# Performance work log

Hardware: AMD Instinct MI355X
Metric: run time of the kernel (lower is better)

## Reference

```python
import jax, jax.numpy as jnp
import numpy as np

IC = 64   # inter_channels
S = 3     # num_subset_S
ST = 2    # num_subset_T


def _bn(x, g, b):
    # BatchNorm2d in eval mode with running_mean=0, running_var=1, eps=1e-5
    return x * (g / jnp.sqrt(1.0 + 1e-5))[:, None, None] + b[:, None, None]


def _c1(x, W, b):
    # 1x1 Conv2d over (N, C, T, V)
    return jnp.einsum('oc,nctv->notv', W, x) + b[None, :, None, None]


def setup_inputs() -> dict:
    key = jax.random.key(0)
    ks = iter(jax.random.split(key, 40))
    r = lambda sh: jax.random.normal(next(ks), sh, dtype=jnp.float32) * 0.05
    N, C, T, V = 64, 128, 64, 25
    d = {}
    d['x'] = jax.random.normal(next(ks), (N, C, T, V), dtype=jnp.float32)
    d['W_ins'] = r((2 * S * IC, C)); d['b_ins'] = r((2 * S * IC,))
    d['alphas'] = jnp.ones((1, S, 1, 1), jnp.float32)
    d['att0s'] = jnp.full((1, S, V, V), 1.0 / V, jnp.float32)
    d['W_outs'] = r((C, S * C)); d['b_outs'] = r((C,))
    d['g_outs'] = jnp.ones((C,), jnp.float32) + r((C,)); d['be_outs'] = r((C,))
    d['W_ffs'] = r((C, C)); d['b_ffs'] = r((C,))
    d['g_ffs'] = jnp.ones((C,), jnp.float32) + r((C,)); d['be_ffs'] = r((C,))
    d['W_int'] = r((4 * ST * IC, C)); d['b_int'] = r((4 * ST * IC,))
    d['alphat_b'] = jnp.ones((1, ST, 1, 1), jnp.float32)
    d['alphat_f'] = jnp.ones((1, ST, 1, 1), jnp.float32)
    d['W_outt'] = r((C, 2 * ST * C)); d['b_outt'] = r((C,))
    d['g_outt'] = jnp.ones((C,), jnp.float32) + r((C,)); d['be_outt'] = r((C,))
    d['W_fft'] = r((C, C)); d['b_fft'] = r((C,))
    d['g_fft'] = jnp.ones((C,), jnp.float32) + r((C,)); d['be_fft'] = r((C,))
    d['W_tcn'] = r((C, C, 7, 1)); d['b_tcn'] = r((C,))
    d['g_tcn'] = jnp.ones((C,), jnp.float32) + r((C,)); d['be_tcn'] = r((C,))
    return d


def reference(x, W_ins, b_ins, alphas, att0s, W_outs, b_outs, g_outs, be_outs,
              W_ffs, b_ffs, g_ffs, be_ffs, W_int, b_int, alphat_b, alphat_f,
              W_outt, b_outt, g_outt, be_outt, W_fft, b_fft, g_fft, be_fft,
              W_tcn, b_tcn, g_tcn, be_tcn):
    N, C, T, V = x.shape
    lrelu = lambda a: jax.nn.leaky_relu(a, 0.1)

    # ---- spatial attention ----
    qk = _c1(x, W_ins, b_ins).reshape(N, 2 * S, IC, T, V)
    q, k = qk[:, :S], qk[:, S:]
    att = jnp.tanh(jnp.einsum('nsctu,nsctv->nsuv', q, k) / (IC * T)) * alphas + att0s
    y = jnp.einsum('nctu,nsuv->nsctv', x, att).reshape(N, S * C, T, V)
    y = lrelu(x + _bn(_c1(y, W_outs, b_outs), g_outs, be_outs))   # out_nets + residual
    y = lrelu(x + _bn(_c1(y, W_ffs, b_ffs), g_ffs, be_ffs))       # ff_nets + residual (downs2 = identity)

    # ---- directed temporal attention ----
    bm = jnp.triu(jnp.ones((T, T), x.dtype))  # backward mask
    fm = bm.T                                  # forward mask (tril)
    qk = _c1(y, W_int, b_int).reshape(N, 4 * ST, IC, T, V)
    q_f, q_b = qk[:, :ST], qk[:, ST:2 * ST]
    k_f, k_b = qk[:, 2 * ST:3 * ST], qk[:, 3 * ST:]
    att_b = jnp.tanh(jnp.einsum('nsctv,nscqv->nstq', q_b, k_b) / (IC * V)) * alphat_b * bm
    att_f = jnp.tanh(jnp.einsum('nsctv,nscqv->nstq', q_f, k_f) / (IC * V)) * alphat_f * fm
    z_f = jnp.einsum('nctv,nstq->nscqv', y, att_f).reshape(N, ST * C, T, V)
    z_b = jnp.einsum('nctv,nstq->nscqv', y, att_b).reshape(N, ST * C, T, V)
    z = jnp.concatenate([z_f, z_b], axis=1)                        # (N, 2*ST*C, T, V)
    z = lrelu(y + _bn(_c1(z, W_outt, b_outt), g_outt, be_outt))    # out_nett + residual
    z = lrelu(y + _bn(_c1(z, W_fft, b_fft), g_fft, be_fft))        # ff_nett + residual

    # ---- TCN extension: (7,1) temporal conv + BN + residual ----
    z1 = jax.lax.conv_general_dilated(z, W_tcn, (1, 1), ((3, 3), (0, 0)),
                                      dimension_numbers=('NCHW', 'OIHW', 'NCHW'))
    z1 = _bn(z1 + b_tcn[None, :, None, None] - b_tcn[None, :, None, None] + b_tcn[None, :, None, None], g_tcn, be_tcn) if False else _bn(z1 + b_tcn[None, :, None, None], g_tcn, be_tcn)
    z = lrelu(z + z1)
    return z
```

## Files before the change

### kernel.cpp

```cpp
#include <hip/hip_runtime.h>

#define BNSC 0.99999500003749963f

typedef _Float16 f16;
typedef _Float16 f16x8 __attribute__((ext_vector_type(8)));
typedef float    f32x4 __attribute__((ext_vector_type(4)));

static __device__ __forceinline__ float lrelu_f(float a) { return a >= 0.0f ? a : 0.1f * a; }

static __device__ __forceinline__ void xcd_swz(int& bx, int& by, int& bz) {
    const int GX = gridDim.x, GY = gridDim.y, GZ = gridDim.z;
    if (((GX * GZ) & 7) == 0) {
        const int lin = blockIdx.x + GX * (blockIdx.y + GY * blockIdx.z);
        const int xcd = lin & 7;
        const int rest = lin >> 3;
        by = rest % GY;
        const int g = (rest / GY) * 8 + xcd;
        bx = g % GX;
        bz = g / GX;
    } else {
        bx = blockIdx.x; by = blockIdx.y; bz = blockIdx.z;
    }
}

__global__ __launch_bounds__(256) void prep_w_k(
    const float* __restrict__ Wins, const float* __restrict__ Wouts,
    const float* __restrict__ Wffs, const float* __restrict__ Wint,
    const float* __restrict__ Woutt, const float* __restrict__ Wfft,
    const float* __restrict__ Wtcn, f16* __restrict__ dst)
{
    int i = blockIdx.x * 256 + threadIdx.x;
    int o = 0;
    if (i < 49152) { dst[o + i] = (f16)Wins[i];  return; } i -= 49152; o += 49152;
    if (i < 49152) { dst[o + i] = (f16)Wouts[i]; return; } i -= 49152; o += 49152;
    if (i < 16384) { dst[o + i] = (f16)Wffs[i];  return; } i -= 16384; o += 16384;
    if (i < 65536) { dst[o + i] = (f16)Wint[i];  return; } i -= 65536; o += 65536;
    if (i < 65536) { dst[o + i] = (f16)Woutt[i]; return; } i -= 65536; o += 65536;
    if (i < 16384) { dst[o + i] = (f16)Wfft[i];  return; } i -= 16384; o += 16384;
    if (i < 114688) {
        int tau = i / 16384, rem = i - tau * 16384;
        dst[o + i] = (f16)Wtcn[(size_t)rem * 7 + tau];
    }
}

__global__ __launch_bounds__(256) void x_to_T_k(const float* __restrict__ x,
                                                f16* __restrict__ xT, f16* __restrict__ xBp)
{
    __shared__ float L[64 * 68];
    const int n = blockIdx.z, tv0 = blockIdx.x * 64, c0 = blockIdx.y * 64;
    const int tid = threadIdx.x;
    const int cc = tid >> 4, tv4 = (tid & 15) * 4;
    f16* xBn = xBp + (size_t)n * 262144;
    #pragma unroll
    for (int p = 0; p < 4; ++p) {
        const int c = cc + p * 16;
        float4 v = *(const float4*)&x[((size_t)n * 128 + c0 + c) * 1600 + tv0 + tv4];
        *(float4*)&L[c * 68 + tv4] = v;
        const float vv[4] = {v.x, v.y, v.z, v.w};
        #pragma unroll
        for (int e = 0; e < 4; ++e) {
            const int tvg = tv0 + tv4 + e;
            const int t = tvg / 25, u = tvg - t * 25;
            xBn[(size_t)(c0 + c) * 2048 + t * 32 + u] = (f16)vv[e];
        }
    }
    __syncthreads();
    const int tv = tid & 63, cb = (tid >> 6) * 16;
    f16x8 o0, o1;
    #pragma unroll
    for (int i = 0; i < 8; ++i) o0[i] = (f16)L[(cb + i) * 68 + tv];
    #pragma unroll
    for (int i = 0; i < 8; ++i) o1[i] = (f16)L[(cb + 8 + i) * 68 + tv];
    f16* dst = &xT[((size_t)n * 1600 + tv0 + tv) * 128 + c0 + cb];
    *(f16x8*)dst = o0;
    *(f16x8*)(dst + 8) = o1;
}

__global__ __launch_bounds__(256) void T_to_out_k(const f16* __restrict__ oT, float* __restrict__ out)
{
    __shared__ float L[128 * 69];
    const int n = blockIdx.z, tv0 = blockIdx.x * 64;
    const int tid = threadIdx.x;
    #pragma unroll
    for (int p = 0; p < 4; ++p) {
        int idx = tid + p * 256;
        int tv = idx >> 4, c8 = (idx & 15) * 8;
        f16x8 v = *(const f16x8*)&oT[((size_t)n * 1600 + tv0 + tv) * 128 + c8];
        #pragma unroll
        for (int i = 0; i < 8; ++i) L[(c8 + i) * 69 + tv] = (float)v[i];
    }
    __syncthreads();
    const int c = tid >> 1, tvb = (tid & 1) * 32;
    #pragma unroll
    for (int j = 0; j < 8; ++j) {
        float4 o;
        o.x = L[c * 69 + tvb + j * 4 + 0];
        o.y = L[c * 69 + tvb + j * 4 + 1];
        o.z = L[c * 69 + tvb + j * 4 + 2];
        o.w = L[c * 69 + tvb + j * 4 + 3];
        *(float4*)&out[((size_t)n * 128 + c) * 1600 + tv0 + tvb + j * 4] = o;
    }
}

template<int EPI>
__global__ __launch_bounds__(256) void gemm_t_k(
    const f16* __restrict__ A,
    const f16* __restrict__ W,
    const float* __restrict__ bias,
    const float* __restrict__ g, const float* __restrict__ be,
    const f16* __restrict__ res,
    f16* __restrict__ out,
    int K, int M)
{
    __shared__ __align__(16) char smem[34816];
    f16* As = (f16*)smem;
    f16* Bs = (f16*)(smem + 17408);
    float* Ss = (float*)smem;
    int bx, by, bz;
    xcd_swz(bx, by, bz);
    const int n = bz, tv0 = bx * 64, m0 = by * 64;
    const int tid = threadIdx.x;
    const int w = tid >> 6, lane = tid & 63;
    const int wr = w >> 1, wc = w & 1;
    const int lg = lane >> 4, lr = lane & 15;
    const int srow = tid >> 3, scol = (tid & 7) * 16;
    const f16* An = A + (size_t)n * 1600 * K;
    f32x4 acc[2][2] = {};

    for (int k0 = 0; k0 < K; k0 += 128) {
        const f16* ar0 = An + (size_t)(tv0 + srow) * K + k0 + scol;
        const f16* ar1 = An + (size_t)(tv0 + srow + 32) * K + k0 + scol;
        const f16* br0 = W + (size_t)(m0 + srow) * K + k0 + scol;
        const f16* br1 = W + (size_t)(m0 + srow + 32) * K + k0 + scol;
        uint4 a0 = *(const uint4*)ar0, a1 = *(const uint4*)(ar0 + 8);
        uint4 a2 = *(const uint4*)ar1, a3 = *(const uint4*)(ar1 + 8);
        uint4 b0 = *(const uint4*)br0, b1 = *(const uint4*)(br0 + 8);
        uint4 b2 = *(const uint4*)br1, b3 = *(const uint4*)(br1 + 8);
        __syncthreads();
        *(uint4*)&As[srow * 136 + scol] = a0;
        *(uint4*)&As[srow * 136 + scol + 8] = a1;
        *(uint4*)&As[(srow + 32) * 136 + scol] = a2;
        *(uint4*)&As[(srow + 32) * 136 + scol + 8] = a3;
        *(uint4*)&Bs[srow * 136 + scol] = b0;
        *(uint4*)&Bs[srow * 136 + scol + 8] = b1;
        *(uint4*)&Bs[(srow + 32) * 136 + scol] = b2;
        *(uint4*)&Bs[(srow + 32) * 136 + scol + 8] = b3;
        __syncthreads();
        #pragma unroll
        for (int kb = 0; kb < 128; kb += 32) {
            f16x8 af0 = *(const f16x8*)&As[(wr * 32 + lr) * 136 + kb + lg * 8];
            f16x8 af1 = *(const f16x8*)&As[(wr * 32 + 16 + lr) * 136 + kb + lg * 8];
            f16x8 bf0 = *(const f16x8*)&Bs[(wc * 32 + lr) * 136 + kb + lg * 8];
            f16x8 bf1 = *(const f16x8*)&Bs[(wc * 32 + 16 + lr) * 136 + kb + lg * 8];
            acc[0][0] = __builtin_amdgcn_mfma_f32_16x16x32_f16(af0, bf0, acc[0][0], 0, 0, 0);
            acc[0][1] = __builtin_amdgcn_mfma_f32_16x16x32_f16(af0, bf1, acc[0][1], 0, 0, 0);
            acc[1][0] = __builtin_amdgcn_mfma_f32_16x16x32_f16(af1, bf0, acc[1][0], 0, 0, 0);
            acc[1][1] = __builtin_amdgcn_mfma_f32_16x16x32_f16(af1, bf1, acc[1][1], 0, 0, 0);
        }
        __syncthreads();
    }
    #pragma unroll
    for (int fi = 0; fi < 2; ++fi)
        #pragma unroll
        for (int fj = 0; fj < 2; ++fj)
            #pragma unroll
            for (int rr = 0; rr < 4; ++rr)
                Ss[(wr * 32 + fi * 16 + lg * 4 + rr) * 68 + wc * 32 + fj * 16 + lr] = acc[fi][fj][rr];
    __syncthreads();
    const int tvl = tid >> 2, mq = (tid & 3) * 16;
    const int tv = tv0 + tvl;
    const int m  = m0 + mq;
    float vals[16];
    #pragma unroll
    for (int j = 0; j < 4; ++j)
        *(float4*)&vals[j * 4] = *(const float4*)&Ss[tvl * 68 + mq + j * 4];
    float bi[16];
    #pragma unroll
    for (int j = 0; j < 4; ++j) *(float4*)&bi[j * 4] = *(const float4*)&bias[m + j * 4];
    if (EPI == 1) {
        float gg[16], bb[16];
        #pragma unroll
        for (int j = 0; j < 4; ++j) {
            *(float4*)&gg[j * 4] = *(const float4*)&g[m + j * 4];
            *(float4*)&bb[j * 4] = *(const float4*)&be[m + j * 4];
        }
        const f16* rp = res + ((size_t)n * 1600 + tv) * M + m;
        f16x8 r0 = *(const f16x8*)rp;
        f16x8 r1 = *(const f16x8*)(rp + 8);
        #pragma unroll
        for (int j = 0; j < 16; ++j) {
            float r = (float)((j < 8) ? r0[j & 7] : r1[j & 7]);
            vals[j] = lrelu_f(r + (vals[j] + bi[j]) * (gg[j] * BNSC) + bb[j]);
        }
    } else {
        #pragma unroll
        for (int j = 0; j < 16; ++j) vals[j] += bi[j];
    }
    f16x8 o0, o1;
    #pragma unroll
    for (int j = 0; j < 8; ++j) { o0[j] = (f16)vals[j]; o1[j] = (f16)vals[8 + j]; }
    f16* op = out + ((size_t)n * 1600 + tv) * M + m;
    *(f16x8*)op = o0;
    *(f16x8*)(op + 8) = o1;
}

__global__ __launch_bounds__(256) void tcn_T_k(
    const f16* __restrict__ z2T,
    const f16* __restrict__ W7,
    const float* __restrict__ bias, const float* __restrict__ g,
    const float* __restrict__ be, f16* __restrict__ outT)
{
    __shared__ __align__(16) char smem[34816];
    f16* As = (f16*)smem;
    f16* Bs = (f16*)(smem + 17408);
    float* Ss = (float*)smem;
    int bx, by, bz;
    xcd_swz(bx, by, bz);
    const int n = bz, tv0 = bx * 64, m0 = by * 64;
    const int tid = threadIdx.x;
    const int w = tid >> 6, lane = tid & 63;
    const int wr = w >> 1, wc = w & 1;
    const int lg = lane >> 4, lr = lane & 15;
    const int srow = tid >> 3, scol = (tid & 7) * 16;
    const f16* Zn = z2T + (size_t)n * 204800;
    f32x4 acc[2][2] = {};

    for (int tau = 0; tau < 7; ++tau) {
        const int shift = (tau - 3) * 25;
        const f16* Wt = W7 + tau * 16384;
        const int gr0 = tv0 + srow + shift;
        const int gr1 = gr0 + 32;
        uint4 a0 = make_uint4(0,0,0,0), a1 = a0, a2 = a0, a3 = a0;
        if (gr0 >= 0 && gr0 < 1600) {
            const f16* p = Zn + (size_t)gr0 * 128 + scol;
            a0 = *(const uint4*)p; a1 = *(const uint4*)(p + 8);
        }
        if (gr1 >= 0 && gr1 < 1600) {
            const f16* p = Zn + (size_t)gr1 * 128 + scol;
            a2 = *(const uint4*)p; a3 = *(const uint4*)(p + 8);
        }
        const f16* br0 = Wt + (size_t)(m0 + srow) * 128 + scol;
        const f16* br1 = Wt + (size_t)(m0 + srow + 32) * 128 + scol;
        uint4 b0 = *(const uint4*)br0, b1 = *(const uint4*)(br0 + 8);
        uint4 b2 = *(const uint4*)br1, b3 = *(const uint4*)(br1 + 8);
        __syncthreads();
        *(uint4*)&As[srow * 136 + scol] = a0;
        *(uint4*)&As[srow * 136 + scol + 8] = a1;
        *(uint4*)&As[(srow + 32) * 136 + scol] = a2;
        *(uint4*)&As[(srow + 32) * 136 + scol + 8] = a3;
        *(uint4*)&Bs[srow * 136 + scol] = b0;
        *(uint4*)&Bs[srow * 136 + scol + 8] = b1;
        *(uint4*)&Bs[(srow + 32) * 136 + scol] = b2;
        *(uint4*)&Bs[(srow + 32) * 136 + scol + 8] = b3;
        __syncthreads();
        #pragma unroll
        for (int kb = 0; kb < 128; kb += 32) {
            f16x8 af0 = *(const f16x8*)&As[(wr * 32 + lr) * 136 + kb + lg * 8];
            f16x8 af1 = *(const f16x8*)&As[(wr * 32 + 16 + lr) * 136 + kb + lg * 8];
            f16x8 bf0 = *(const f16x8*)&Bs[(wc * 32 + lr) * 136 + kb + lg * 8];
            f16x8 bf1 = *(const f16x8*)&Bs[(wc * 32 + 16 + lr) * 136 + kb + lg * 8];
            acc[0][0] = __builtin_amdgcn_mfma_f32_16x16x32_f16(af0, bf0, acc[0][0], 0, 0, 0);
            acc[0][1] = __builtin_amdgcn_mfma_f32_16x16x32_f16(af0, bf1, acc[0][1], 0, 0, 0);
            acc[1][0] = __builtin_amdgcn_mfma_f32_16x16x32_f16(af1, bf0, acc[1][0], 0, 0, 0);
            acc[1][1] = __builtin_amdgcn_mfma_f32_16x16x32_f16(af1, bf1, acc[1][1], 0, 0, 0);
        }
        __syncthreads();
    }
    #pragma unroll
    for (int fi = 0; fi < 2; ++fi)
        #pragma unroll
        for (int fj = 0; fj < 2; ++fj)
            #pragma unroll
            for (int rr = 0; rr < 4; ++rr)
                Ss[(wr * 32 + fi * 16 + lg * 4 + rr) * 68 + wc * 32 + fj * 16 + lr] = acc[fi][fj][rr];
    __syncthreads();
    const int tvl = tid >> 2, mq = (tid & 3) * 16;
    const int tv = tv0 + tvl;
    const int m  = m0 + mq;
    float vals[16], bi[16], gg[16], bb[16];
    #pragma unroll
    for (int j = 0; j < 4; ++j) {
        *(float4*)&vals[j * 4] = *(const float4*)&Ss[tvl * 68 + mq + j * 4];
        *(float4*)&bi[j * 4]   = *(const float4*)&bias[m + j * 4];
        *(float4*)&gg[j * 4]   = *(const float4*)&g[m + j * 4];
        *(float4*)&bb[j * 4]   = *(const float4*)&be[m + j * 4];
    }
    const f16* rp = Zn + (size_t)tv * 128 + m;
    f16x8 r0 = *(const f16x8*)rp;
    f16x8 r1 = *(const f16x8*)(rp + 8);
    #pragma unroll
    for (int j = 0; j < 16; ++j) {
        float r = (float)((j < 8) ? r0[j & 7] : r1[j & 7]);
        vals[j] = lrelu_f(r + (vals[j] + bi[j]) * (gg[j] * BNSC) + bb[j]);
    }
    f16x8 o0, o1;
    #pragma unroll
    for (int j = 0; j < 8; ++j) { o0[j] = (f16)vals[j]; o1[j] = (f16)vals[8 + j]; }
    f16* op = outT + ((size_t)n * 1600 + tv) * 128 + m;
    *(f16x8*)op = o0;
    *(f16x8*)(op + 8) = o1;
}

__global__ __launch_bounds__(256) void att_s_mfma_k(
    const f16* __restrict__ QKT,
    float* __restrict__ P)
{
    __shared__ float Lred[4][1024];
    const int n = blockIdx.x / 24;
    const int rs = blockIdx.x % 24;
    const int s = rs >> 3, tc = rs & 7;
    const int tid = threadIdx.x;
    const int w = tid >> 6, lane = tid & 63;
    const int lg = lane >> 4, lr = lane & 15;
    const int qc = s * 64, kc = 192 + s * 64;
    const f16* Qn = QKT + (size_t)n * 1600 * 384;
    f32x4 acc[2][2] = {};

    #pragma unroll
    for (int tt = 0; tt < 2; ++tt) {
        const int t = tc * 8 + w * 2 + tt;
        const size_t rbase = (size_t)t * 25;
        #pragma unroll
        for (int kb = 0; kb < 2; ++kb) {
            f16x8 a[2] = {}, b[2] = {};
            #pragma unroll
            for (int rt = 0; rt < 2; ++rt) {
                const int u = rt * 16 + lr;
                if (u < 25) {
                    const f16* rp = Qn + (rbase + u) * 384;
                    a[rt] = *(const f16x8*)(rp + qc + kb * 32 + lg * 8);
                    b[rt] = *(const f16x8*)(rp + kc + kb * 32 + lg * 8);
                }
            }
            #pragma unroll
            for (int rt = 0; rt < 2; ++rt)
                #pragma unroll
                for (int ct = 0; ct < 2; ++ct)
                    acc[rt][ct] = __builtin_amdgcn_mfma_f32_16x16x32_f16(a[rt], b[ct], acc[rt][ct], 0, 0, 0);
        }
    }
    #pragma unroll
    for (int rt = 0; rt < 2; ++rt)
        #pragma unroll
        for (int ct = 0; ct < 2; ++ct)
            #pragma unroll
            for (int rr = 0; rr < 4; ++rr) {
                const int u = rt * 16 + lg * 4 + rr;
                const int v = ct * 16 + lr;
                Lred[w][u * 32 + v] = acc[rt][ct][rr];
            }
    __syncthreads();
    float* Pp = P + (((size_t)n * 3 + s) * 8 + tc) * 1024;
    for (int i = tid; i < 1024; i += 256)
        Pp[i] = Lred[0][i] + Lred[1][i] + Lred[2][i] + Lred[3][i];
}

__global__ __launch_bounds__(256) void att_s_fin_k(
    const float* __restrict__ P, const float* __restrict__ alphas,
    const float* __restrict__ att0s, float* __restrict__ att)
{
    const int n = blockIdx.x / 3, s = blockIdx.x % 3;
    const float* Pp = P + ((size_t)n * 3 + s) * 8192;
    const float al = alphas[s];
    for (int p = threadIdx.x; p < 625; p += 256) {
        const int u = p / 25, v = p - u * 25;
        float sum = 0.f;
        #pragma unroll
        for (int tc = 0; tc < 8; ++tc) sum += Pp[tc * 1024 + u * 32 + v];
        att[((size_t)n * 3 + s) * 625 + p] = tanhf(sum * (1.0f / 4096.0f)) * al + att0s[s * 625 + p];
    }
}

__global__ __launch_bounds__(256) void att_t_mfma_k(
    const f16* __restrict__ QKT,
    const float* __restrict__ alphat_b, const float* __restrict__ alphat_f,
    float* __restrict__ att)
{
    __shared__ f16 Qs[64 * 72];
    __shared__ f16 Ks[64 * 72];
    const int n = blockIdx.x >> 2, r = blockIdx.x & 3;
    const int br = r >> 1, s = r & 1;
    const int qg = ((br == 0) ? s : 2 + s) * 64;
    const int kg = ((br == 0) ? 4 + s : 6 + s) * 64;
    const f16* Qn = QKT + (size_t)n * 1600 * 512;
    const int tid = threadIdx.x;
    const int w = tid >> 6, lane = tid & 63;
    const int lg = lane >> 4, lr = lane & 15;
    const int srow = tid >> 2, scol = (tid & 3) * 16;
    f32x4 acc[4] = {};

    for (int v = 0; v < 25; ++v) {
        const f16* rowp = Qn + (size_t)(srow * 25 + v) * 512;
        uint4 q0 = *(const uint4*)(rowp + qg + scol);
        uint4 q1 = *(const uint4*)(rowp + qg + scol + 8);
        uint4 k0 = *(const uint4*)(rowp + kg + scol);
        uint4 k1 = *(const uint4*)(rowp + kg + scol + 8);
        __syncthreads();
        *(uint4*)&Qs[srow * 72 + scol] = q0;
        *(uint4*)&Qs[srow * 72 + scol + 8] = q1;
        *(uint4*)&Ks[srow * 72 + scol] = k0;
        *(uint4*)&Ks[srow * 72 + scol + 8] = k1;
        __syncthreads();
        #pragma unroll
        for (int kb = 0; kb < 2; ++kb) {
            f16x8 a = *(const f16x8*)&Qs[(w * 16 + lr) * 72 + kb * 32 + lg * 8];
            #pragma unroll
            for (int ct = 0; ct < 4; ++ct) {
                f16x8 b = *(const f16x8*)&Ks[(ct * 16 + lr) * 72 + kb * 32 + lg * 8];
                acc[ct] = __builtin_amdgcn_mfma_f32_16x16x32_f16(a, b, acc[ct], 0, 0, 0);
            }
        }
    }
    const float al = (br == 0) ? alphat_f[s] : alphat_b[s];
    float* ap = att + (((size_t)n * 2 + br) * 2 + s) * 4096;
    #pragma unroll
    for (int ct = 0; ct < 4; ++ct) {
        #pragma unroll
        for (int rr = 0; rr < 4; ++rr) {
            const int t = w * 16 + lg * 4 + rr;
            const int q = ct * 16 + lr;
            const bool keep = (br == 0) ? (t >= q) : (q >= t);
            ap[t * 64 + q] = keep ? tanhf(acc[ct][rr] * (1.0f / 1600.0f)) * al : 0.0f;
        }
    }
}

__global__ __launch_bounds__(256) void apply_s_mfma_k(
    const f16* __restrict__ xBp,
    const float* __restrict__ att,
    f16* __restrict__ y1T)
{
    __shared__ f16 As[3 * 32 * 48];
    const int n = blockIdx.x >> 6, t = blockIdx.x & 63;
    const int tid = threadIdx.x;
    const int w = tid >> 6, lane = tid & 63;
    const int lg = lane >> 4, lr = lane & 15;
    const float* an = att + (size_t)n * 1875;
    for (int i = tid; i < 3 * 32 * 48; i += 256) {
        int s = i / 1536, r2 = i - s * 1536;
        int v = r2 / 48, u = r2 - v * 48;
        As[i] = (v < 25 && u < 25) ? (f16)an[s * 625 + u * 25 + v] : (f16)0.f;
    }
    __syncthreads();
    const f16* Bn = xBp + (size_t)n * 262144 + (size_t)t * 32;
    f16x8 bf[2];
    #pragma unroll
    for (int ct = 0; ct < 2; ++ct)
        bf[ct] = *(const f16x8*)(Bn + (size_t)(w * 32 + ct * 16 + lr) * 2048 + lg * 8);
    #pragma unroll
    for (int s = 0; s < 3; ++s) {
        f32x4 acc[2][2] = {};
        #pragma unroll
        for (int vt = 0; vt < 2; ++vt) {
            f16x8 a = *(const f16x8*)&As[s * 1536 + (vt * 16 + lr) * 48 + lg * 8];
            #pragma unroll
            for (int ct = 0; ct < 2; ++ct)
                acc[vt][ct] = __builtin_amdgcn_mfma_f32_16x16x32_f16(a, bf[ct], acc[vt][ct], 0, 0, 0);
        }
        #pragma unroll
        for (int vt = 0; vt < 2; ++vt)
            #pragma unroll
            for (int ct = 0; ct < 2; ++ct)
                #pragma unroll
                for (int rr = 0; rr < 4; ++rr) {
                    const int v = vt * 16 + lg * 4 + rr;
                    if (v < 25) {
                        const int c = w * 32 + ct * 16 + lr;
                        y1T[((size_t)n * 1600 + t * 25 + v) * 384 + s * 128 + c] = (f16)acc[vt][ct][rr];
                    }
                }
    }
}

__global__ __launch_bounds__(256) void t_to_B_k(
    const f16* __restrict__ y2T, f16* __restrict__ Y2B)
{
    __shared__ f16 L[64 * 136];
    const int n = blockIdx.x, v = blockIdx.y;
    const f16* Yn = y2T + (size_t)n * 204800;
    const int tid = threadIdx.x;
    for (int i = tid; i < 1024; i += 256) {
        int t = i >> 4, c8 = (i & 15) * 8;
        *(f16x8*)&L[t * 136 + c8] = *(const f16x8*)&Yn[(size_t)(t * 25 + v) * 128 + c8];
    }
    __syncthreads();
    const int c = tid >> 1, t0 = (tid & 1) * 32;
    f16* dst = Y2B + ((size_t)n * 25 + v) * 8192 + (size_t)c * 64 + t0;
    #pragma unroll
    for (int j = 0; j < 4; ++j) {
        f16x8 o;
        #pragma unroll
        for (int e = 0; e < 8; ++e) o[e] = L[(t0 + j * 8 + e) * 136 + c];
        *(f16x8*)(dst + j * 8) = o;
    }
}

__global__ __launch_bounds__(256) void apply_t_mfma_k(
    const f16* __restrict__ Y2B,
    const float* __restrict__ att,
    f16* __restrict__ zT)
{
    __shared__ f16 AsT[4][64 * 72];
    const int n = blockIdx.x;
    const int by = blockIdx.y;
    const int vg = by >> 1;
    const int ch = (by & 1) * 64;
    const int tid = threadIdx.x;
    const int w = tid >> 6, lane = tid & 63;
    const int lg = lane >> 4, lr = lane & 15;
    const float* ap = att + (size_t)n * 4 * 4096;
    for (int i = tid; i < 4 * 4096; i += 256) {
        int r = i >> 12, rem = i & 4095;
        int t = rem >> 6, q = rem & 63;
        AsT[r][q * 72 + t] = (f16)ap[i];
    }
    __syncthreads();
    f16x8 af[4][2];
    #pragma unroll
    for (int qt = 0; qt < 4; ++qt)
        #pragma unroll
        for (int kb = 0; kb < 2; ++kb)
            af[qt][kb] = *(const f16x8*)&AsT[w][(qt * 16 + lr) * 72 + kb * 32 + lg * 8];

    for (int vi = 0; vi < 5; ++vi) {
        const int v = vg * 5 + vi;
        const f16* Bv = Y2B + ((size_t)n * 25 + v) * 8192 + (size_t)ch * 64;
        f32x4 acc[4][4] = {};
        #pragma unroll
        for (int kb = 0; kb < 2; ++kb)
            #pragma unroll
            for (int ct = 0; ct < 4; ++ct) {
                f16x8 bf = *(const f16x8*)(Bv + (size_t)(ct * 16 + lr) * 64 + kb * 32 + lg * 8);
                #pragma unroll
                for (int qt = 0; qt < 4; ++qt)
                    acc[qt][ct] = __builtin_amdgcn_mfma_f32_16x16x32_f16(af[qt][kb], bf, acc[qt][ct], 0, 0, 0);
            }
        #pragma unroll
        for (int qt = 0; qt < 4; ++qt)
            #pragma unroll
            for (int ct = 0; ct < 4; ++ct)
                #pragma unroll
                for (int rr = 0; rr < 4; ++rr) {
                    const int q = qt * 16 + lg * 4 + rr;
                    const int c = ch + ct * 16 + lr;
                    zT[((size_t)n * 1600 + q * 25 + v) * 512 + w * 128 + c] = (f16)acc[qt][ct][rr];
                }
    }
}

extern "C" void kernel_launch(void* const* d_in, const int* in_sizes, int n_in,
                              void* d_out, int out_size, void* d_ws, size_t ws_size,
                              hipStream_t stream) {
    const float* x       = (const float*)d_in[0];
    const float* W_ins   = (const float*)d_in[1];
    const float* b_ins   = (const float*)d_in[2];
    const float* alphas  = (const float*)d_in[3];
    const float* att0s   = (const float*)d_in[4];
    const float* W_outs  = (const float*)d_in[5];
    const float* b_outs  = (const float*)d_in[6];
    const float* g_outs  = (const float*)d_in[7];
    const float* be_outs = (const float*)d_in[8];
    const float* W_ffs   = (const float*)d_in[9];
    const float* b_ffs   = (const float*)d_in[10];
    const float* g_ffs   = (const float*)d_in[11];
    const float* be_ffs  = (const float*)d_in[12];
    const float* W_int   = (const float*)d_in[13];
    const float* b_int   = (const float*)d_in[14];
    const float* alphat_b= (const float*)d_in[15];
    const float* alphat_f= (const float*)d_in[16];
    const float* W_outt  = (const float*)d_in[17];
    const float* b_outt  = (const float*)d_in[18];
    const float* g_outt  = (const float*)d_in[19];
    const float* be_outt = (const float*)d_in[20];
    const float* W_fft   = (const float*)d_in[21];
    const float* b_fft   = (const float*)d_in[22];
    const float* g_fft   = (const float*)d_in[23];
    const float* be_fft  = (const float*)d_in[24];
    const float* W_tcn   = (const float*)d_in[25];
    const float* b_tcn   = (const float*)d_in[26];
    const float* g_tcn   = (const float*)d_in[27];
    const float* be_tcn  = (const float*)d_in[28];

    f16* wf = (f16*)d_ws;
    f16* W_ins16  = wf;
    f16* W_outs16 = wf + 49152;
    f16* W_ffs16  = wf + 98304;
    f16* W_int16  = wf + 114688;
    f16* W_outt16 = wf + 180224;
    f16* W_fft16  = wf + 245760;
    f16* W_tcn16  = wf + 262144;
    const size_t wbytes = 753664;

    const size_t perN = (819200ull + 3ull * 204800ull + 204800ull + 262144ull) * 2ull;
    int Nc = 64;
    while (Nc > 4 && wbytes + (size_t)Nc * perN > ws_size) Nc >>= 1;

    f16* A   = (f16*)((char*)d_ws + wbytes);
    f16* B   = A   + (size_t)Nc * 819200;
    f16* C   = B   + (size_t)Nc * 204800;
    f16* D   = C   + (size_t)Nc * 204800;
    f16* Y2B = D   + (size_t)Nc * 204800;
    f16* xBp = Y2B + (size_t)Nc * 204800;
    float* P    = (float*)Y2B;
    float* attS = (float*)Y2B + (size_t)Nc * 24576;
    float* attT = (float*)B;

    prep_w_k<<<1472, 256, 0, stream>>>(W_ins, W_outs, W_ffs, W_int, W_outt, W_fft, W_tcn, wf);

    for (int n0 = 0; n0 < 64; n0 += Nc) {
        const float* xc = x + (size_t)n0 * 204800;
        float* outc     = (float*)d_out + (size_t)n0 * 204800;

        x_to_T_k<<<dim3(25, 2, Nc), 256, 0, stream>>>(xc, D, xBp);
        gemm_t_k<0><<<dim3(25, 6, Nc), 256, 0, stream>>>(D, W_ins16, b_ins, nullptr, nullptr,
                                                         nullptr, A, 128, 384);
        att_s_mfma_k<<<dim3(24 * Nc), 256, 0, stream>>>(A, P);
        att_s_fin_k<<<dim3(3 * Nc), 256, 0, stream>>>(P, alphas, att0s, attS);
        apply_s_mfma_k<<<dim3(64 * Nc), 256, 0, stream>>>(xBp, attS, A);
        gemm_t_k<1><<<dim3(25, 2, Nc), 256, 0, stream>>>(A, W_outs16, b_outs, g_outs, be_outs,
                                                         D, B, 384, 128);
        gemm_t_k<1><<<dim3(25, 2, Nc), 256, 0, stream>>>(B, W_ffs16, b_ffs, g_ffs, be_ffs,
                                                         D, C, 128, 128);
        t_to_B_k<<<dim3(Nc, 25), 256, 0, stream>>>(C, Y2B);
        gemm_t_k<0><<<dim3(25, 8, Nc), 256, 0, stream>>>(C, W_int16, b_int, nullptr, nullptr,
                                                         nullptr, A, 128, 512);
        att_t_mfma_k<<<dim3(4 * Nc), 256, 0, stream>>>(A, alphat_b, alphat_f, attT);
        apply_t_mfma_k<<<dim3(Nc, 10), 256, 0, stream>>>(Y2B, attT, A);
        gemm_t_k<1><<<dim3(25, 2, Nc), 256, 0, stream>>>(A, W_outt16, b_outt, g_outt, be_outt,
                                                         C, B, 512, 128);
        gemm_t_k<1><<<dim3(25, 2, Nc), 256, 0, stream>>>(B, W_fft16, b_fft, g_fft, be_fft,
                                                         C, D, 128, 128);
        tcn_T_k<<<dim3(25, 2, Nc), 256, 0, stream>>>(D, W_tcn16, b_tcn, g_tcn, be_tcn, A);
        T_to_out_k<<<dim3(25, 1, Nc), 256, 0, stream>>>(A, outc);
    }
}
```

Measured before the change: 431.0 us.

## Fuse out-projection and feed-forward 1x1 GEMMs into one kernel per branch

Adds a fused2_k kernel that computes the out-net GEMM with its BN, residual and leaky-ReLU epilogue, keeps the 64x128 intermediate tile in shared memory, then runs the feed-forward GEMM and its epilogue in the same block. It is used for both the spatial and the temporal branch, replacing two gemm_t_k launches each. This removes the intermediate global write and read plus two launches. In exchange each block now covers all 128 output channels, so the grid is half as large (25 x Nc blocks), the GEMM K-step shrinks to 64 with no double buffering, and register pressure rises from 8 accumulators per thread.

```diff
diff --git a/kernel.cpp b/kernel.cpp
--- a/kernel.cpp
+++ b/kernel.cpp
@@ -104,12 +104,10 @@
 
 template<int EPI>
 __global__ __launch_bounds__(256) void gemm_t_k(
-    const f16* __restrict__ A,
-    const f16* __restrict__ W,
+    const f16* __restrict__ A, const f16* __restrict__ W,
     const float* __restrict__ bias,
     const float* __restrict__ g, const float* __restrict__ be,
-    const f16* __restrict__ res,
-    f16* __restrict__ out,
+    const f16* __restrict__ res, f16* __restrict__ out,
     int K, int M)
 {
     __shared__ __align__(16) char smem[34816];
@@ -204,9 +202,164 @@
     *(f16x8*)(op + 8) = o1;
 }
 
+template<int K1>
+__global__ __launch_bounds__(256) void fused2_k(
+    const f16* __restrict__ Ain,
+    const f16* __restrict__ W1,
+    const float* __restrict__ b1, const float* __restrict__ g1, const float* __restrict__ be1,
+    const f16* __restrict__ W2,
+    const float* __restrict__ b2, const float* __restrict__ g2, const float* __restrict__ be2,
+    const f16* __restrict__ res,
+    f16* __restrict__ out)
+{
+    __shared__ __align__(16) char smem[35840];
+    f16* As1  = (f16*)smem;
+    f16* Bs1  = (f16*)(smem + 9216);
+    float* Ss = (float*)smem;
+    f16* Ys   = (f16*)smem;
+    f16* Bs2  = (f16*)(smem + 17408);
+    int bx, by, bz;
+    xcd_swz(bx, by, bz);
+    const int n = bz, tv0 = bx * 64;
+    const int tid = threadIdx.x;
+    const int w = tid >> 6, lane = tid & 63;
+    const int wr = w >> 1, wc = w & 1;
+    const int lg = lane >> 4, lr = lane & 15;
+    const int srow = tid >> 3, sc = (tid & 7) * 8;
+    const f16* An = Ain + (size_t)n * 1600 * K1;
+    const f16* rn = res + ((size_t)n * 1600 + tv0) * 128;
+
+    f32x4 acc[2][4] = {};
+    for (int k0 = 0; k0 < K1; k0 += 64) {
+        uint4 a0 = *(const uint4*)(An + (size_t)(tv0 + srow) * K1 + k0 + sc);
+        uint4 a1 = *(const uint4*)(An + (size_t)(tv0 + srow + 32) * K1 + k0 + sc);
+        uint4 w0 = *(const uint4*)(W1 + (size_t)srow * K1 + k0 + sc);
+        uint4 w1v = *(const uint4*)(W1 + (size_t)(srow + 32) * K1 + k0 + sc);
+        uint4 w2v = *(const uint4*)(W1 + (size_t)(srow + 64) * K1 + k0 + sc);
+        uint4 w3v = *(const uint4*)(W1 + (size_t)(srow + 96) * K1 + k0 + sc);
+        __syncthreads();
+        *(uint4*)&As1[srow * 72 + sc] = a0;
+        *(uint4*)&As1[(srow + 32) * 72 + sc] = a1;
+        *(uint4*)&Bs1[srow * 72 + sc] = w0;
+        *(uint4*)&Bs1[(srow + 32) * 72 + sc] = w1v;
+        *(uint4*)&Bs1[(srow + 64) * 72 + sc] = w2v;
+        *(uint4*)&Bs1[(srow + 96) * 72 + sc] = w3v;
+        __syncthreads();
+        #pragma unroll
+        for (int kb = 0; kb < 64; kb += 32) {
+            f16x8 af0 = *(const f16x8*)&As1[(wr * 32 + lr) * 72 + kb + lg * 8];
+            f16x8 af1 = *(const f16x8*)&As1[(wr * 32 + 16 + lr) * 72 + kb + lg * 8];
+            #pragma unroll
+            for (int ft = 0; ft < 4; ++ft) {
+                f16x8 bf = *(const f16x8*)&Bs1[(wc * 64 + ft * 16 + lr) * 72 + kb + lg * 8];
+                acc[0][ft] = __builtin_amdgcn_mfma_f32_16x16x32_f16(af0, bf, acc[0][ft], 0, 0, 0);
+                acc[1][ft] = __builtin_amdgcn_mfma_f32_16x16x32_f16(af1, bf, acc[1][ft], 0, 0, 0);
+            }
+        }
+        __syncthreads();
+    }
+    #pragma unroll
+    for (int fi = 0; fi < 2; ++fi)
+        #pragma unroll
+        for (int ft = 0; ft < 4; ++ft)
+            #pragma unroll
+            for (int rr = 0; rr < 4; ++rr)
+                Ss[(wr * 32 + fi * 16 + lg * 4 + rr) * 132 + wc * 64 + ft * 16 + lr] = acc[fi][ft][rr];
+    __syncthreads();
+    const int tvl = tid >> 2, q4 = (tid & 3) * 16;
+    f16x8 yh[4];
+    #pragma unroll
+    for (int mh = 0; mh < 2; ++mh) {
+        const int mq = mh * 64 + q4;
+        float vals[16], bb[16], gg[16], eb[16];
+        #pragma unroll
+        for (int j = 0; j < 4; ++j) {
+            *(float4*)&vals[j * 4] = *(const float4*)&Ss[tvl * 132 + mq + j * 4];
+            *(float4*)&bb[j * 4]   = *(const float4*)&b1[mq + j * 4];
+            *(float4*)&gg[j * 4]   = *(const float4*)&g1[mq + j * 4];
+            *(float4*)&eb[j * 4]   = *(const float4*)&be1[mq + j * 4];
+        }
+        const f16* rp = rn + (size_t)tvl * 128 + mq;
+        f16x8 r0 = *(const f16x8*)rp, r1 = *(const f16x8*)(rp + 8);
+        #pragma unroll
+        for (int j = 0; j < 16; ++j) {
+            float r = (float)((j < 8) ? r0[j & 7] : r1[j & 7]);
+            vals[j] = lrelu_f(r + (vals[j] + bb[j]) * (gg[j] * BNSC) + eb[j]);
+        }
+        #pragma unroll
+        for (int j = 0; j < 8; ++j) {
+            yh[mh * 2][j]     = (f16)vals[j];
+            yh[mh * 2 + 1][j] = (f16)vals[8 + j];
+        }
+    }
+    __syncthreads();
+    *(f16x8*)&Ys[tvl * 136 + q4]          = yh[0];
+    *(f16x8*)&Ys[tvl * 136 + q4 + 8]      = yh[1];
+    *(f16x8*)&Ys[tvl * 136 + 64 + q4]     = yh[2];
+    *(f16x8*)&Ys[tvl * 136 + 64 + q4 + 8] = yh[3];
+
+    f32x4 acc2[2][4] = {};
+    for (int k2 = 0; k2 < 128; k2 += 64) {
+        uint4 w0 = *(const uint4*)(W2 + (size_t)srow * 128 + k2 + sc);
+        uint4 w1v = *(const uint4*)(W2 + (size_t)(srow + 32) * 128 + k2 + sc);
+        uint4 w2v = *(const uint4*)(W2 + (size_t)(srow + 64) * 128 + k2 + sc);
+        uint4 w3v = *(const uint4*)(W2 + (size_t)(srow + 96) * 128 + k2 + sc);
+        __syncthreads();
+        *(uint4*)&Bs2[srow * 72 + sc] = w0;
+        *(uint4*)&Bs2[(srow + 32) * 72 + sc] = w1v;
+        *(uint4*)&Bs2[(srow + 64) * 72 + sc] = w2v;
+        *(uint4*)&Bs2[(srow + 96) * 72 + sc] = w3v;
+        __syncthreads();
+        #pragma unroll
+        for (int kb = 0; kb < 64; kb += 32) {
+            f16x8 af0 = *(const f16x8*)&Ys[(wr * 32 + lr) * 136 + k2 + kb + lg * 8];
+            f16x8 af1 = *(const f16x8*)&Ys[(wr * 32 + 16 + lr) * 136 + k2 + kb + lg * 8];
+            #pragma unroll
+            for (int ft = 0; ft < 4; ++ft) {
+                f16x8 bf = *(const f16x8*)&Bs2[(wc * 64 + ft * 16 + lr) * 72 + kb + lg * 8];
+                acc2[0][ft] = __builtin_amdgcn_mfma_f32_16x16x32_f16(af0, bf, acc2[0][ft], 0, 0, 0);
+                acc2[1][ft] = __builtin_amdgcn_mfma_f32_16x16x32_f16(af1, bf, acc2[1][ft], 0, 0, 0);
+            }
+        }
+    }
+    __syncthreads();
+    #pragma unroll
+    for (int fi = 0; fi < 2; ++fi)
+        #pragma unroll
+        for (int ft = 0; ft < 4; ++ft)
+            #pragma unroll
+            for (int rr = 0; rr < 4; ++rr)
+                Ss[(wr * 32 + fi * 16 + lg * 4 + rr) * 132 + wc * 64 + ft * 16 + lr] = acc2[fi][ft][rr];
+    __syncthreads();
+    f16* op = out + ((size_t)n * 1600 + tv0 + tvl) * 128;
+    #pragma unroll
+    for (int mh = 0; mh < 2; ++mh) {
+        const int mq = mh * 64 + q4;
+        float vals[16], bb[16], gg[16], eb[16];
+        #pragma unroll
+        for (int j = 0; j < 4; ++j) {
+            *(float4*)&vals[j * 4] = *(const float4*)&Ss[tvl * 132 + mq + j * 4];
+            *(float4*)&bb[j * 4]   = *(const float4*)&b2[mq + j * 4];
+            *(float4*)&gg[j * 4]   = *(const float4*)&g2[mq + j * 4];
+            *(float4*)&eb[j * 4]   = *(const float4*)&be2[mq + j * 4];
+        }
+        const f16* rp = rn + (size_t)tvl * 128 + mq;
+        f16x8 r0 = *(const f16x8*)rp, r1 = *(const f16x8*)(rp + 8);
+        #pragma unroll
+        for (int j = 0; j < 16; ++j) {
+            float r = (float)((j < 8) ? r0[j & 7] : r1[j & 7]);
+            vals[j] = lrelu_f(r + (vals[j] + bb[j]) * (gg[j] * BNSC) + eb[j]);
+        }
+        f16x8 o0, o1;
+        #pragma unroll
+        for (int j = 0; j < 8; ++j) { o0[j] = (f16)vals[j]; o1[j] = (f16)vals[8 + j]; }
+        *(f16x8*)(op + mq) = o0;
+        *(f16x8*)(op + mq + 8) = o1;
+    }
+}
+
 __global__ __launch_bounds__(256) void tcn_T_k(
-    const f16* __restrict__ z2T,
-    const f16* __restrict__ W7,
+    const f16* __restrict__ z2T, const f16* __restrict__ W7,
     const float* __restrict__ bias, const float* __restrict__ g,
     const float* __restrict__ be, f16* __restrict__ outT)
 {
@@ -302,8 +455,7 @@
 }
 
 __global__ __launch_bounds__(256) void att_s_mfma_k(
-    const f16* __restrict__ QKT,
-    float* __restrict__ P)
+    const f16* __restrict__ QKT, float* __restrict__ P)
 {
     __shared__ float Lred[4][1024];
     const int n = blockIdx.x / 24;
@@ -426,9 +578,7 @@
 }
 
 __global__ __launch_bounds__(256) void apply_s_mfma_k(
-    const f16* __restrict__ xBp,
-    const float* __restrict__ att,
-    f16* __restrict__ y1T)
+    const f16* __restrict__ xBp, const float* __restrict__ att, f16* __restrict__ y1T)
 {
     __shared__ f16 As[3 * 32 * 48];
     const int n = blockIdx.x >> 6, t = blockIdx.x & 63;
@@ -496,9 +646,7 @@
 }
 
 __global__ __launch_bounds__(256) void apply_t_mfma_k(
-    const f16* __restrict__ Y2B,
-    const float* __restrict__ att,
-    f16* __restrict__ zT)
+    const f16* __restrict__ Y2B, const float* __restrict__ att, f16* __restrict__ zT)
 {
     __shared__ f16 AsT[4][64 * 72];
     const int n = blockIdx.x;
@@ -617,19 +765,15 @@
         att_s_mfma_k<<<dim3(24 * Nc), 256, 0, stream>>>(A, P);
         att_s_fin_k<<<dim3(3 * Nc), 256, 0, stream>>>(P, alphas, att0s, attS);
         apply_s_mfma_k<<<dim3(64 * Nc), 256, 0, stream>>>(xBp, attS, A);
-        gemm_t_k<1><<<dim3(25, 2, Nc), 256, 0, stream>>>(A, W_outs16, b_outs, g_outs, be_outs,
-                                                         D, B, 384, 128);
-        gemm_t_k<1><<<dim3(25, 2, Nc), 256, 0, stream>>>(B, W_ffs16, b_ffs, g_ffs, be_ffs,
-                                                         D, C, 128, 128);
+        fused2_k<384><<<dim3(25, 1, Nc), 256, 0, stream>>>(A, W_outs16, b_outs, g_outs, be_outs,
+                                                           W_ffs16, b_ffs, g_ffs, be_ffs, D, C);
         t_to_B_k<<<dim3(Nc, 25), 256, 0, stream>>>(C, Y2B);
         gemm_t_k<0><<<dim3(25, 8, Nc), 256, 0, stream>>>(C, W_int16, b_int, nullptr, nullptr,
                                                          nullptr, A, 128, 512);
         att_t_mfma_k<<<dim3(4 * Nc), 256, 0, stream>>>(A, alphat_b, alphat_f, attT);
         apply_t_mfma_k<<<dim3(Nc, 10), 256, 0, stream>>>(Y2B, attT, A);
-        gemm_t_k<1><<<dim3(25, 2, Nc), 256, 0, stream>>>(A, W_outt16, b_outt, g_outt, be_outt,
-                                                         C, B, 512, 128);
-        gemm_t_k<1><<<dim3(25, 2, Nc), 256, 0, stream>>>(B, W_fft16, b_fft, g_fft, be_fft,
-                                                         C, D, 128, 128);
+        fused2_k<512><<<dim3(25, 1, Nc), 256, 0, stream>>>(A, W_outt16, b_outt, g_outt, be_outt,
+                                                           W_fft16, b_fft, g_fft, be_fft, C, D);
         tcn_T_k<<<dim3(25, 2, Nc), 256, 0, stream>>>(D, W_tcn16, b_tcn, g_tcn, be_tcn, A);
         T_to_out_k<<<dim3(25, 1, Nc), 256, 0, stream>>>(A, outc);
     }
```

New measurement: 431.2 us. About the same (+0.0%).
